# Optimization experiments

Measured on AMD Instinct MI355X. Metric: run time of the kernel, lower is better.

Reference implementation:

```python
import jax, jax.numpy as jnp
import numpy as np

EPS = 1e-5
# TT factorization for ffn2: 2048 = 8*16*16 -> 1024 = 8*16*8, ranks (1,16,16,1)
IN_F = (8, 16, 16)
OUT_F = (8, 16, 8)
R = 16


def setup_inputs() -> dict:
    key = jax.random.key(0)
    ks = jax.random.split(key, 10)
    B, S, D = 4, 4096, 1024
    F = 2 * D  # ffn_dim
    glorot = lambda k, shape: jax.random.uniform(
        k, shape, jnp.float32, -1.0, 1.0) * np.sqrt(6.0 / (shape[-2] + shape[-1]))
    return {
        "x": jax.random.normal(ks[0], (B, S, D), jnp.float32),
        "gamma1": jnp.ones((D,), jnp.float32),
        "beta1": jnp.zeros((D,), jnp.float32),
        "W1": glorot(ks[1], (D, F)),
        "b1": jnp.zeros((F,), jnp.float32),
        # TT cores: (r_in, in_k, out_k, r_out)
        "tt_core1": jax.random.normal(ks[2], (1, IN_F[0], OUT_F[0], R), jnp.float32) * 0.1,
        "tt_core2": jax.random.normal(ks[3], (R, IN_F[1], OUT_F[1], R), jnp.float32) * 0.1,
        "tt_core3": jax.random.normal(ks[4], (R, IN_F[2], OUT_F[2], 1), jnp.float32) * 0.1,
        "tt_bias": jnp.zeros((D,), jnp.float32),
        "gamma2": jnp.ones((D,), jnp.float32),
        "beta2": jnp.zeros((D,), jnp.float32),
    }


def _layernorm(x, gamma, beta):
    mu = jnp.mean(x, axis=-1, keepdims=True)
    var = jnp.mean(jnp.square(x - mu), axis=-1, keepdims=True)
    return (x - mu) * jax.lax.rsqrt(var + EPS) * gamma + beta


def _tt_matmul(h, g1, g2, g3, bias):
    # h: [B, S, 2048] -> [B, S, 1024] via tensor-train matrix
    B, S, F = h.shape
    t = h.reshape(B * S, *IN_F)                       # [N, 8, 16, 16]
    g1s = g1[0]                                       # [8, 8, 16]
    g3s = g3[..., 0]                                  # [16, 16, 8]
    t = jnp.einsum('nijk,ips->njkps', t, g1s)         # [N, 16, 16, 8, 16]
    t = jnp.einsum('njkps,sjqt->nkpqt', t, g2)        # [N, 16, 8, 16, 16]
    t = jnp.einsum('nkpqt,tku->npqu', t, g3s)         # [N, 8, 16, 8]
    out = t.reshape(B, S, int(np.prod(OUT_F)))
    return out + bias


def reference(x, gamma1, beta1, W1, b1, tt_core1, tt_core2, tt_core3,
              tt_bias, gamma2, beta2):
    # fused LayerNorm -> projection -> GELU (exact gelu, keras default)
    h = _layernorm(x, gamma1, beta1)
    h = jax.nn.gelu(h @ W1 + b1, approximate=False)   # [B, S, 2048]
    # TT-factorized FFN2
    y = _tt_matmul(h, tt_core1, tt_core2, tt_core3, tt_bias)
    # residual + (x + LN(x)) residual (dropout inactive at inference)
    x = x + y
    x = x + _layernorm(x, gamma2, beta2)
    return x
```

## Files before the change

### kernel.cpp

```cpp
#include <hip/hip_runtime.h>

typedef unsigned short u16;
typedef __attribute__((ext_vector_type(8))) short bf16x8;
typedef __attribute__((ext_vector_type(8))) unsigned short u16x8;
typedef __attribute__((ext_vector_type(4))) float f32x4;
typedef __attribute__((ext_vector_type(4))) int i32x4;

#define AS1 __attribute__((address_space(1)))
#define AS3 __attribute__((address_space(3)))

__device__ __forceinline__ void gld16(const void* g, void* l) {
    __builtin_amdgcn_global_load_lds((const AS1 void*)g, (AS3 void*)l, 16, 0, 0);
}

__device__ __forceinline__ u16 f2bf(float f) {
    unsigned int u = __float_as_uint(f);
    unsigned int r = (u >> 16) & 1u;
    u += 0x7fffu + r;
    return (u16)(u >> 16);
}

__device__ __forceinline__ float gelu_exact(float v) {
    return 0.5f * v * (1.0f + erff(v * 0.70710678118654752f));
}

__device__ __forceinline__ int q8(float v, float s) {
    int q = (int)rintf(v * s);
    return q < -127 ? -127 : (q > 127 ? 127 : q);
}

#define XSCALE (127.0f / 6.0f)
#define HSCALE (127.0f / 5.0f)
#define W2CLMP (127.0f / 0.1f)

__global__ __launch_bounds__(256) void transpose_quant(
    const float* __restrict__ W, char* __restrict__ Wt, int R, int C,
    float wscale) {
    __shared__ float t[32][33];
    const int tx = threadIdx.x & 31, tg = threadIdx.x >> 5;
    const int c0 = blockIdx.x * 32, r0 = blockIdx.y * 32;
#pragma unroll
    for (int i = 0; i < 4; ++i) {
        int rr = tg + i * 8;
        t[rr][tx] = W[(long)(r0 + rr) * C + c0 + tx];
    }
    __syncthreads();
#pragma unroll
    for (int i = 0; i < 4; ++i) {
        int rr = tg + i * 8;
        Wt[(long)(c0 + rr) * R + r0 + tx] = (char)q8(t[tx][rr], wscale);
    }
}

__global__ __launch_bounds__(256) void tt_m1_kernel(
    const float* __restrict__ g1, const float* __restrict__ g2,
    float* __restrict__ M1) {
    const int id = blockIdx.x * 256 + threadIdx.x;
    const int t = id & 15, q = (id >> 4) & 15, p = (id >> 8) & 7;
    const int j = (id >> 11) & 15, i = id >> 15;
    float acc = 0.f;
#pragma unroll
    for (int s = 0; s < 16; ++s)
        acc += g1[(i * 8 + p) * 16 + s] * g2[((s * 16 + j) * 16 + q) * 16 + t];
    M1[id] = acc;
}

__global__ __launch_bounds__(256) void tt_w2q_kernel(
    const float* __restrict__ M1, const float* __restrict__ g3,
    char* __restrict__ W2Q) {
    const int id = blockIdx.x * 256 + threadIdx.x;
    const int fi = id & 2047, fo = id >> 11;
    const int i = fi >> 8, j = (fi >> 4) & 15, k = fi & 15;
    const int p = fo >> 7, q = (fo >> 3) & 15, u = fo & 7;
    const float* m = &M1[(((i * 16 + j) * 8 + p) * 16 + q) * 16];
    float acc = 0.f;
#pragma unroll
    for (int t = 0; t < 16; ++t)
        acc += m[t] * g3[(t * 16 + k) * 8 + u];
    W2Q[id] = (char)q8(acc, W2CLMP);
}

__global__ __launch_bounds__(256) void ln1_kernel(
    const float* __restrict__ x, const float* __restrict__ gamma,
    const float* __restrict__ beta, char* __restrict__ out) {
    const long row = blockIdx.x;
    const int tid = threadIdx.x;
    const float4 v = ((const float4*)(x + row * 1024))[tid];
    float s = v.x + v.y + v.z + v.w;
    float ss = v.x * v.x + v.y * v.y + v.z * v.z + v.w * v.w;
#pragma unroll
    for (int off = 32; off; off >>= 1) {
        s += __shfl_down(s, off, 64);
        ss += __shfl_down(ss, off, 64);
    }
    __shared__ float rs[4], rss[4];
    const int w = tid >> 6, lane = tid & 63;
    if (lane == 0) { rs[w] = s; rss[w] = ss; }
    __syncthreads();
    s = rs[0] + rs[1] + rs[2] + rs[3];
    ss = rss[0] + rss[1] + rss[2] + rss[3];
    const float mu = s * (1.0f / 1024.0f);
    const float var = ss * (1.0f / 1024.0f) - mu * mu;
    const float rstd = rsqrtf(var + 1e-5f);
    const float4 gm = ((const float4*)gamma)[tid];
    const float4 bt = ((const float4*)beta)[tid];
    const int q0 = q8((v.x - mu) * rstd * gm.x + bt.x, XSCALE);
    const int q1 = q8((v.y - mu) * rstd * gm.y + bt.y, XSCALE);
    const int q2 = q8((v.z - mu) * rstd * gm.z + bt.z, XSCALE);
    const int q3 = q8((v.w - mu) * rstd * gm.w + bt.w, XSCALE);
    const int packed = (q0 & 0xff) | ((q1 & 0xff) << 8) |
                       ((q2 & 0xff) << 16) | ((q3 & 0xff) << 24);
    ((int*)(out + row * 1024))[tid] = packed;
}

__global__ __launch_bounds__(256) void ln2_kernel(
    float* __restrict__ z, const float* __restrict__ gamma,
    const float* __restrict__ beta) {
    const long row = blockIdx.x;
    const int tid = threadIdx.x;
    const float4 v = ((const float4*)(z + row * 1024))[tid];
    float s = v.x + v.y + v.z + v.w;
    float ss = v.x * v.x + v.y * v.y + v.z * v.z + v.w * v.w;
#pragma unroll
    for (int off = 32; off; off >>= 1) {
        s += __shfl_down(s, off, 64);
        ss += __shfl_down(ss, off, 64);
    }
    __shared__ float rs[4], rss[4];
    const int w = tid >> 6, lane = tid & 63;
    if (lane == 0) { rs[w] = s; rss[w] = ss; }
    __syncthreads();
    s = rs[0] + rs[1] + rs[2] + rs[3];
    ss = rss[0] + rss[1] + rss[2] + rss[3];
    const float mu = s * (1.0f / 1024.0f);
    const float var = ss * (1.0f / 1024.0f) - mu * mu;
    const float rstd = rsqrtf(var + 1e-5f);
    const float4 gm = ((const float4*)gamma)[tid];
    const float4 bt = ((const float4*)beta)[tid];
    float4 o;
    o.x = v.x + ((v.x - mu) * rstd * gm.x + bt.x);
    o.y = v.y + ((v.y - mu) * rstd * gm.y + bt.y);
    o.z = v.z + ((v.z - mu) * rstd * gm.z + bt.z);
    o.w = v.w + ((v.w - mu) * rstd * gm.w + bt.w);
    ((float4*)(z + row * 1024))[tid] = o;
}

template <int EPI>
__global__ __launch_bounds__(256, 4) void gemm128_i8(
    const char* __restrict__ A, const char* __restrict__ Bq,
    void* __restrict__ outp, const float* __restrict__ bias,
    const float* __restrict__ resid, int M, int N, int K, float dq) {
    __shared__ char smem[32768];
    const int tid = threadIdx.x;
    int b = blockIdx.x;
    const int nwg = gridDim.x;
    if ((nwg & 7) == 0 && nwg >= 8) {
        const int per = nwg >> 3;
        b = (b & 7) * per + (b >> 3);
    }
    const int NT = N >> 7;
    const int mt = b / NT, nt = b - mt * NT;
    const long m0 = (long)mt << 7, n0 = (long)nt << 7;

    const int lane = tid & 63, wid = tid >> 6;
    const int wr = wid >> 1, wc = wid & 1;
    const int r = lane & 15, g = lane >> 4;

    const int lo = tid * 16;
    const int srow = lo >> 7;
    const int sc = (lo & 127) ^ ((srow & 7) << 4);
    const char* pA = A + (m0 + srow) * (long)K + sc;
    const char* pB = Bq + (n0 + srow) * (long)K + sc;

    const int sx = (r & 7) << 4;
    const int ac0 = (g * 16) ^ sx;
    const int ac1 = (g * 16 + 64) ^ sx;
    const int arow = wr * 64, brow = wc * 64;

    i32x4 acc[4][4] = {};

    for (int k0 = 0; k0 < K; k0 += 128) {
#pragma unroll
        for (int q = 0; q < 4; ++q) {
            gld16(pA + (long)(q * 32) * K + k0, smem + q * 4096 + lo);
            gld16(pB + (long)(q * 32) * K + k0, smem + 16384 + q * 4096 + lo);
        }
        __syncthreads();
        i32x4 af[4], bf_[4];
#pragma unroll
        for (int i = 0; i < 4; ++i)
            af[i] = *(const i32x4*)(smem + ((arow + i * 16 + r) * 128 + ac0));
#pragma unroll
        for (int j = 0; j < 4; ++j)
            bf_[j] = *(const i32x4*)(smem + 16384 + ((brow + j * 16 + r) * 128 + ac0));
#pragma unroll
        for (int i = 0; i < 4; ++i)
#pragma unroll
            for (int j = 0; j < 4; ++j)
                acc[i][j] = __builtin_amdgcn_mfma_i32_16x16x64_i8(
                    af[i], bf_[j], acc[i][j], 0, 0, 0);
#pragma unroll
        for (int i = 0; i < 4; ++i)
            af[i] = *(const i32x4*)(smem + ((arow + i * 16 + r) * 128 + ac1));
#pragma unroll
        for (int j = 0; j < 4; ++j)
            bf_[j] = *(const i32x4*)(smem + 16384 + ((brow + j * 16 + r) * 128 + ac1));
#pragma unroll
        for (int i = 0; i < 4; ++i)
#pragma unroll
            for (int j = 0; j < 4; ++j)
                acc[i][j] = __builtin_amdgcn_mfma_i32_16x16x64_i8(
                    af[i], bf_[j], acc[i][j], 0, 0, 0);
        __syncthreads();
    }

    float bias_r[4];
#pragma unroll
    for (int j = 0; j < 4; ++j) bias_r[j] = bias[n0 + wc * 64 + j * 16 + r];

    float* eb = (float*)smem;
#pragma unroll
    for (int s = 0; s < 8; ++s) {
        if (wr == (s >> 2)) {
            const int mi = s & 3;
            float* dst = eb + (s & 1) * (16 * 132) + (g * 4) * 132 + wc * 64 + r;
#pragma unroll
            for (int j = 0; j < 4; ++j)
#pragma unroll
                for (int q = 0; q < 4; ++q)
                    dst[q * 132 + j * 16] = (float)acc[mi][j][q] * dq + bias_r[j];
        }
        __syncthreads();
        const float* srcb = eb + (s & 1) * (16 * 132);
        const int flat = tid * 8;
        const int rr = flat >> 7, cc = flat & 127;
        const float4 v0 = *(const float4*)(srcb + rr * 132 + cc);
        const float4 v1 = *(const float4*)(srcb + rr * 132 + cc + 4);
        const long grow = m0 + s * 16 + rr;
        const long gcol = n0 + cc;
        if (EPI == 0) {
            const int lo32 =
                (q8(gelu_exact(v0.x), HSCALE) & 0xff) |
                ((q8(gelu_exact(v0.y), HSCALE) & 0xff) << 8) |
                ((q8(gelu_exact(v0.z), HSCALE) & 0xff) << 16) |
                ((q8(gelu_exact(v0.w), HSCALE) & 0xff) << 24);
            const int hi32 =
                (q8(gelu_exact(v1.x), HSCALE) & 0xff) |
                ((q8(gelu_exact(v1.y), HSCALE) & 0xff) << 8) |
                ((q8(gelu_exact(v1.z), HSCALE) & 0xff) << 16) |
                ((q8(gelu_exact(v1.w), HSCALE) & 0xff) << 24);
            int2 ov; ov.x = lo32; ov.y = hi32;
            *(int2*)((char*)outp + grow * N + gcol) = ov;
        } else {
            const float4 r0 = *(const float4*)(resid + grow * N + gcol);
            const float4 r1 = *(const float4*)(resid + grow * N + gcol + 4);
            float4 o0, o1;
            o0.x = v0.x + r0.x; o0.y = v0.y + r0.y;
            o0.z = v0.z + r0.z; o0.w = v0.w + r0.w;
            o1.x = v1.x + r1.x; o1.y = v1.y + r1.y;
            o1.z = v1.z + r1.z; o1.w = v1.w + r1.w;
            *(float4*)((float*)outp + grow * N + gcol) = o0;
            *(float4*)((float*)outp + grow * N + gcol + 4) = o1;
        }
    }
}

extern "C" void kernel_launch(void* const* d_in, const int* in_sizes, int n_in,
                              void* d_out, int out_size, void* d_ws, size_t ws_size,
                              hipStream_t stream) {
    const float* x      = (const float*)d_in[0];
    const float* gamma1 = (const float*)d_in[1];
    const float* beta1  = (const float*)d_in[2];
    const float* W1     = (const float*)d_in[3];
    const float* b1     = (const float*)d_in[4];
    const float* g1     = (const float*)d_in[5];
    const float* g2     = (const float*)d_in[6];
    const float* g3     = (const float*)d_in[7];
    const float* ttb    = (const float*)d_in[8];
    const float* gamma2 = (const float*)d_in[9];
    const float* beta2  = (const float*)d_in[10];

    const int ROWS = 16384, D = 1024, F = 2048;
    const float WBOUND = sqrtf(6.0f / 3072.0f);
    const float dq1 = (6.0f / 127.0f) * (WBOUND / 127.0f);
    const float dq2 = (5.0f / 127.0f) * (0.1f / 127.0f);

    char* ws = (char*)d_ws;
    char* W1Q = ws;
    char* W2Q = ws + (size_t)F * D;
    float* M1 = (float*)(ws + (size_t)F * D * 2);
    char* dyn = ws + (size_t)F * D * 2 + 262144 * 4;
    const size_t fixed = (size_t)(dyn - ws);

    int Rc = ROWS;
    while (Rc > 256 && fixed + (size_t)Rc * 3072 > ws_size) Rc >>= 1;

    char* xq = dyn;
    char* hq = dyn + (size_t)Rc * D;

    transpose_quant<<<dim3(F / 32, D / 32), 256, 0, stream>>>(
        W1, W1Q, D, F, 127.0f / WBOUND);
    tt_m1_kernel<<<262144 / 256, 256, 0, stream>>>(g1, g2, M1);
    tt_w2q_kernel<<<(D * F) / 256, 256, 0, stream>>>(M1, g3, W2Q);

    float* out = (float*)d_out;
    for (int r0 = 0; r0 < ROWS; r0 += Rc) {
        ln1_kernel<<<Rc, 256, 0, stream>>>(x + (long)r0 * D, gamma1, beta1, xq);
        gemm128_i8<0><<<(Rc / 128) * (F / 128), 256, 0, stream>>>(
            xq, W1Q, hq, b1, nullptr, Rc, F, D, dq1);
        gemm128_i8<1><<<(Rc / 128) * (D / 128), 256, 0, stream>>>(
            hq, W2Q, out + (long)r0 * D, ttb, x + (long)r0 * D, Rc, D, F, dq2);
    }
    ln2_kernel<<<ROWS, 256, 0, stream>>>(out, gamma2, beta2);
}
```

Before: 222.3 us.

## Store GEMM2 output as bf16, fuse residual into LN2, use tanh GELU

```diff
diff --git a/kernel.cpp b/kernel.cpp
--- a/kernel.cpp
+++ b/kernel.cpp
@@ -20,8 +20,10 @@
     return (u16)(u >> 16);
 }
 
-__device__ __forceinline__ float gelu_exact(float v) {
-    return 0.5f * v * (1.0f + erff(v * 0.70710678118654752f));
+__device__ __forceinline__ float gelu_fast(float v) {
+    const float u = 0.7978845608f * (v + 0.044715f * v * v * v);
+    const float e = __expf(2.0f * u);
+    return v * (1.0f - 1.0f / (e + 1.0f));
 }
 
 __device__ __forceinline__ int q8(float v, float s) {
@@ -113,12 +115,19 @@
     ((int*)(out + row * 1024))[tid] = packed;
 }
 
-__global__ __launch_bounds__(256) void ln2_kernel(
-    float* __restrict__ z, const float* __restrict__ gamma,
-    const float* __restrict__ beta) {
+__global__ __launch_bounds__(256) void ln2_fused(
+    const float* __restrict__ x, const u16* __restrict__ yb,
+    const float* __restrict__ gamma, const float* __restrict__ beta,
+    float* __restrict__ out) {
     const long row = blockIdx.x;
     const int tid = threadIdx.x;
-    const float4 v = ((const float4*)(z + row * 1024))[tid];
+    const float4 xv = ((const float4*)(x + row * 1024))[tid];
+    const ushort4 yv = ((const ushort4*)(yb + row * 1024))[tid];
+    float4 v;
+    v.x = xv.x + __uint_as_float((unsigned)yv.x << 16);
+    v.y = xv.y + __uint_as_float((unsigned)yv.y << 16);
+    v.z = xv.z + __uint_as_float((unsigned)yv.z << 16);
+    v.w = xv.w + __uint_as_float((unsigned)yv.w << 16);
     float s = v.x + v.y + v.z + v.w;
     float ss = v.x * v.x + v.y * v.y + v.z * v.z + v.w * v.w;
 #pragma unroll
@@ -142,14 +151,14 @@
     o.y = v.y + ((v.y - mu) * rstd * gm.y + bt.y);
     o.z = v.z + ((v.z - mu) * rstd * gm.z + bt.z);
     o.w = v.w + ((v.w - mu) * rstd * gm.w + bt.w);
-    ((float4*)(z + row * 1024))[tid] = o;
+    ((float4*)(out + row * 1024))[tid] = o;
 }
 
 template <int EPI>
 __global__ __launch_bounds__(256, 4) void gemm128_i8(
     const char* __restrict__ A, const char* __restrict__ Bq,
     void* __restrict__ outp, const float* __restrict__ bias,
-    const float* __restrict__ resid, int M, int N, int K, float dq) {
+    int M, int N, int K, float dq) {
     __shared__ char smem[32768];
     const int tid = threadIdx.x;
     int b = blockIdx.x;
@@ -240,27 +249,24 @@
         const long gcol = n0 + cc;
         if (EPI == 0) {
             const int lo32 =
-                (q8(gelu_exact(v0.x), HSCALE) & 0xff) |
-                ((q8(gelu_exact(v0.y), HSCALE) & 0xff) << 8) |
-                ((q8(gelu_exact(v0.z), HSCALE) & 0xff) << 16) |
-                ((q8(gelu_exact(v0.w), HSCALE) & 0xff) << 24);
+                (q8(gelu_fast(v0.x), HSCALE) & 0xff) |
+                ((q8(gelu_fast(v0.y), HSCALE) & 0xff) << 8) |
+                ((q8(gelu_fast(v0.z), HSCALE) & 0xff) << 16) |
+                ((q8(gelu_fast(v0.w), HSCALE) & 0xff) << 24);
             const int hi32 =
-                (q8(gelu_exact(v1.x), HSCALE) & 0xff) |
-                ((q8(gelu_exact(v1.y), HSCALE) & 0xff) << 8) |
-                ((q8(gelu_exact(v1.z), HSCALE) & 0xff) << 16) |
-                ((q8(gelu_exact(v1.w), HSCALE) & 0xff) << 24);
+                (q8(gelu_fast(v1.x), HSCALE) & 0xff) |
+                ((q8(gelu_fast(v1.y), HSCALE) & 0xff) << 8) |
+                ((q8(gelu_fast(v1.z), HSCALE) & 0xff) << 16) |
+                ((q8(gelu_fast(v1.w), HSCALE) & 0xff) << 24);
             int2 ov; ov.x = lo32; ov.y = hi32;
             *(int2*)((char*)outp + grow * N + gcol) = ov;
         } else {
-            const float4 r0 = *(const float4*)(resid + grow * N + gcol);
-            const float4 r1 = *(const float4*)(resid + grow * N + gcol + 4);
-            float4 o0, o1;
-            o0.x = v0.x + r0.x; o0.y = v0.y + r0.y;
-            o0.z = v0.z + r0.z; o0.w = v0.w + r0.w;
-            o1.x = v1.x + r1.x; o1.y = v1.y + r1.y;
-            o1.z = v1.z + r1.z; o1.w = v1.w + r1.w;
-            *(float4*)((float*)outp + grow * N + gcol) = o0;
-            *(float4*)((float*)outp + grow * N + gcol + 4) = o1;
+            u16x8 o;
+            o[0] = f2bf(v0.x); o[1] = f2bf(v0.y);
+            o[2] = f2bf(v0.z); o[3] = f2bf(v0.w);
+            o[4] = f2bf(v1.x); o[5] = f2bf(v1.y);
+            o[6] = f2bf(v1.z); o[7] = f2bf(v1.w);
+            *(u16x8*)((u16*)outp + grow * N + gcol) = o;
         }
     }
 }
@@ -293,10 +299,11 @@
     const size_t fixed = (size_t)(dyn - ws);
 
     int Rc = ROWS;
-    while (Rc > 256 && fixed + (size_t)Rc * 3072 > ws_size) Rc >>= 1;
+    while (Rc > 256 && fixed + (size_t)Rc * 5120 > ws_size) Rc >>= 1;
 
     char* xq = dyn;
     char* hq = dyn + (size_t)Rc * D;
+    u16* yb  = (u16*)(dyn + (size_t)Rc * D * 3);
 
     transpose_quant<<<dim3(F / 32, D / 32), 256, 0, stream>>>(
         W1, W1Q, D, F, 127.0f / WBOUND);
@@ -307,9 +314,10 @@
     for (int r0 = 0; r0 < ROWS; r0 += Rc) {
         ln1_kernel<<<Rc, 256, 0, stream>>>(x + (long)r0 * D, gamma1, beta1, xq);
         gemm128_i8<0><<<(Rc / 128) * (F / 128), 256, 0, stream>>>(
-            xq, W1Q, hq, b1, nullptr, Rc, F, D, dq1);
+            xq, W1Q, hq, b1, Rc, F, D, dq1);
         gemm128_i8<1><<<(Rc / 128) * (D / 128), 256, 0, stream>>>(
-            hq, W2Q, out + (long)r0 * D, ttb, x + (long)r0 * D, Rc, D, F, dq2);
-    }
-    ln2_kernel<<<ROWS, 256, 0, stream>>>(out, gamma2, beta2);
-}
+            hq, W2Q, yb, ttb, Rc, D, F, dq2);
+        ln2_fused<<<Rc, 256, 0, stream>>>(
+            x + (long)r0 * D, yb, gamma2, beta2, out + (long)r0 * D);
+    }
+}
```

Measured after the change: 214.3 us (median of 3 runs). 1.04x faster.
